# Kernel tuning notes

Hardware: AMD Instinct MI355X
Metric: run time of the kernel (lower is better)

## Reference

```python
import math
import jax, jax.numpy as jnp
import numpy as np

THETA = 10000.0

def _rope_rotate(x, pos):
    # x: [N,H,T,d] with d even; pos: [T] (int or float positions)
    d = x.shape[-1]
    freqs = THETA ** (-jnp.arange(0, d, 2, dtype=jnp.float32) / d)      # [d/2]
    ang = pos.astype(jnp.float32)[:, None] * freqs                       # [T, d/2]
    cos, sin = jnp.cos(ang), jnp.sin(ang)                                # broadcast over N,H
    x1, x2 = x[..., 0::2], x[..., 1::2]                                  # interleaved pairs
    r1 = x1 * cos - x2 * sin
    r2 = x1 * sin + x2 * cos
    return jnp.stack([r1, r2], axis=-1).reshape(x.shape)

def _apply_rope_2d(q, k, pos_h, pos_w):
    # axial 2D RoPE: first half of head_dim rotated by pos_h, second half by pos_w
    dh = q.shape[-1]
    half = dh // 2
    q = jnp.concatenate([_rope_rotate(q[..., :half], pos_h),
                         _rope_rotate(q[..., half:], pos_w)], axis=-1)
    k = jnp.concatenate([_rope_rotate(k[..., :half], pos_h),
                         _rope_rotate(k[..., half:], pos_w)], axis=-1)
    return q, k

def setup_inputs() -> dict:
    key = jax.random.key(0)
    ks = jax.random.split(key, 6)
    N, T, D, H = 4, 2048, 512, 8
    GH, GW = 64, 32  # 64x32 token grid, GH*GW == T
    x = jax.random.normal(ks[0], (N, T, D), dtype=jnp.float32)
    idx = jnp.arange(T, dtype=jnp.int32)
    pos_h = idx // GW
    pos_w = idx % GW
    scale_in = 1.0 / math.sqrt(D)
    w_qkv = jax.random.normal(ks[1], (D, 3 * D), dtype=jnp.float32) * scale_in
    w_proj = jax.random.normal(ks[2], (D, D), dtype=jnp.float32) * scale_in
    b_proj = jnp.zeros((D,), dtype=jnp.float32)
    return {"x": x, "pos_h": pos_h, "pos_w": pos_w,
            "w_qkv": w_qkv, "w_proj": w_proj, "b_proj": b_proj}

def reference(x, pos_h, pos_w, w_qkv, w_proj, b_proj):
    N, T, D = x.shape
    H = 8
    Dh = D // H
    qkv = x @ w_qkv                                   # [N,T,3D]
    q, k, v = jnp.split(qkv, 3, axis=-1)
    def to_heads(t):
        return t.reshape(N, T, H, Dh).transpose(0, 2, 1, 3)  # [N,H,T,Dh]
    q, k, v = to_heads(q), to_heads(k), to_heads(v)
    q, k = _apply_rope_2d(q, k, pos_h, pos_w)
    attn = jnp.einsum('nhtd,nhsd->nhts', q, k) * (1.0 / math.sqrt(Dh))  # [N,H,T,T]
    p = jax.nn.softmax(attn, axis=-1)
    o = jnp.einsum('nhts,nhsd->nhtd', p, v)           # [N,H,T,Dh]
    o = o.transpose(0, 2, 1, 3).reshape(N, T, D)
    return o @ w_proj + b_proj
```

## Files before the change

### kernel.cpp

```cpp
#include <hip/hip_runtime.h>

typedef __attribute__((ext_vector_type(4))) float f32x4;
typedef __attribute__((ext_vector_type(8))) _Float16 f16x8;
typedef __attribute__((ext_vector_type(2))) __fp16 fp16x2_raw;
typedef __attribute__((ext_vector_type(4))) unsigned int u32x4;
typedef __attribute__((ext_vector_type(2))) unsigned int u32x2;

#define MFMA_F16(a, b, c) __builtin_amdgcn_mfma_f32_16x16x32_f16((a), (b), (c), 0, 0, 0)

__device__ __forceinline__ unsigned int pkrtz(float a, float b) {
  union { fp16x2_raw h; unsigned int u; } v;
  v.h = __builtin_amdgcn_cvt_pkrtz(a, b);
  return v.u;
}

__device__ __forceinline__ float fexp2(float x) {
#if __has_builtin(__builtin_amdgcn_exp2f)
  return __builtin_amdgcn_exp2f(x);
#else
  float r;
  asm("v_exp_f32 %0, %1" : "=v"(r) : "v"(x));
  return r;
#endif
}
__device__ __forceinline__ float fsin_rev(float x) {
#if __has_builtin(__builtin_amdgcn_sinf)
  return __builtin_amdgcn_sinf(x);
#else
  float r; asm("v_sin_f32 %0, %1" : "=v"(r) : "v"(x)); return r;
#endif
}
__device__ __forceinline__ float fcos_rev(float x) {
#if __has_builtin(__builtin_amdgcn_cosf)
  return __builtin_amdgcn_cosf(x);
#else
  float r; asm("v_cos_f32 %0, %1" : "=v"(r) : "v"(x)); return r;
#endif
}

typedef const __attribute__((address_space(1))) unsigned int ga_u32_t;
typedef __attribute__((address_space(3))) unsigned int ls_u32_t;
__device__ __forceinline__ void gload16(const void* g, void* l) {
  __builtin_amdgcn_global_load_lds((ga_u32_t*)g, (ls_u32_t*)l, 16, 0, 0);
}

__device__ __forceinline__ void inv_swz64(int seg, int lane, int& r, int& ch) {
  int r_hi = seg * 8 + (lane >> 3);
  int r0 = ((lane >> 2) & 1) ^ ((r_hi >> 1) & 1);
  r = (r_hi << 1) | r0;
  ch = (lane & 3) ^ (r & 3);
}

__global__ __launch_bounds__(256)
void k_prep_x(const float* __restrict__ in, _Float16* __restrict__ out) {
  int i = (blockIdx.x * 256 + threadIdx.x) * 4;
  f32x4 v = *(const f32x4*)(in + i);
  u32x2 p;
  p.x = pkrtz(v[0], v[1]);
  p.y = pkrtz(v[2], v[3]);
  *(u32x2*)(out + i) = p;
}

__global__ __launch_bounds__(256)
void k_prep_w(const float* __restrict__ in, _Float16* __restrict__ out, int N) {
  __shared__ float t[64][65];
  const int tid = threadIdx.x;
  const int bn = blockIdx.x * 64, bk = blockIdx.y * 64;
  #pragma unroll
  for (int it = 0; it < 16; ++it) {
    int idx = it * 256 + tid;
    int kk = idx >> 6, nn = idx & 63;
    t[kk][nn] = in[(bk + kk) * N + bn + nn];
  }
  __syncthreads();
  #pragma unroll
  for (int it = 0; it < 16; ++it) {
    int idx = it * 256 + tid;
    int nn = idx >> 6, kk = idx & 63;
    out[(bn + nn) * 512 + bk + kk] = (_Float16)t[kk][nn];
  }
}

__global__ __launch_bounds__(256, 3)
void k_gemm_qkv(const _Float16* __restrict__ xh,
                const _Float16* __restrict__ wT,
                const int* __restrict__ pos_h,
                const int* __restrict__ pos_w,
                _Float16* __restrict__ qh,
                _Float16* __restrict__ kh,
                _Float16* __restrict__ vT) {
  __shared__ char As[8192], Bs[8192];
  const int tid = threadIdx.x;
  const int lane = tid & 63, w = tid >> 6;
  const int lr = lane & 15, g = lane >> 4;
  const int m0 = blockIdx.y * 128;
  const int n0 = blockIdx.x * 128;
  const int wr = w >> 1, wc = w & 1;

  const _Float16* asrc[2];
  const _Float16* bsrc[2];
  #pragma unroll
  for (int c = 0; c < 2; ++c) {
    int seg = w * 2 + c, r, ch;
    inv_swz64(seg, lane, r, ch);
    asrc[c] = xh + (size_t)(m0 + r) * 512 + ch * 8;
    bsrc[c] = wT + (size_t)(n0 + r) * 512 + ch * 8;
  }

  f32x4 acc[4][4];
  #pragma unroll
  for (int i = 0; i < 4; ++i)
    #pragma unroll
    for (int j = 0; j < 4; ++j) acc[i][j] = (f32x4){0.f, 0.f, 0.f, 0.f};

  for (int kt = 0; kt < 16; ++kt) {
    const int k0 = kt * 32;
    __syncthreads();
    #pragma unroll
    for (int c = 0; c < 2; ++c) {
      gload16(asrc[c] + k0, As + (w * 2 + c) * 1024);
      gload16(bsrc[c] + k0, Bs + (w * 2 + c) * 1024);
    }
    __syncthreads();

    f16x8 af[4], bf[4];
    #pragma unroll
    for (int mi = 0; mi < 4; ++mi) {
      int r = 64 * wr + 16 * mi + lr;
      af[mi] = *(const f16x8*)(As + (((r << 6) + (g << 4)) ^ ((r & 7) << 4)));
    }
    #pragma unroll
    for (int nj = 0; nj < 4; ++nj) {
      int r = 64 * wc + 16 * nj + lr;
      bf[nj] = *(const f16x8*)(Bs + (((r << 6) + (g << 4)) ^ ((r & 7) << 4)));
    }
    __builtin_amdgcn_s_setprio(1);
    #pragma unroll
    for (int mi = 0; mi < 4; ++mi)
      #pragma unroll
      for (int nj = 0; nj < 4; ++nj)
        acc[mi][nj] = MFMA_F16(af[mi], bf[nj], acc[mi][nj]);
    __builtin_amdgcn_s_setprio(0);
  }

  #pragma unroll
  for (int mi = 0; mi < 4; ++mi) {
    const int r0f = m0 + 64 * wr + 16 * mi + 4 * g;
    const int n = r0f >> 11;
    const int t = r0f & 2047;
    #pragma unroll
    for (int nj = 0; nj < 4; ++nj) {
      const int c = n0 + 64 * wc + 16 * nj + lr;
      const int mat = c >> 9;
      const int hh = (c >> 6) & 7;
      const int dh = c & 63;
      f32x4 v = acc[mi][nj];
      if (mat == 2) {
        int tperm = (t & ~31) + 8 * ((t >> 2) & 3) + 4 * ((t >> 4) & 1);
        u32x2 pk2;
        pk2.x = pkrtz(v[0], v[1]);
        pk2.y = pkrtz(v[2], v[3]);
        *(u32x2*)(vT + (size_t)((n * 8 + hh) * 64 + dh) * 2048 + tperm) = pk2;
      } else {
        const int p = (dh & 31) >> 1;
        const float freq_rev = fexp2((float)p * -0.8304820237218405f) * 0.15915494309189535f;
        const int odd = lane & 1;
        const int* posArr = (dh < 32) ? pos_h : pos_w;
        _Float16* dst = mat ? kh : qh;
        const float scale = mat ? 1.0f : 0.125f * 1.44269504088896f;
        #pragma unroll
        for (int i = 0; i < 4; ++i) {
          float val = v[i];
          float oth = __shfl_xor(val, 1);
          float ar = (float)posArr[t + i] * freq_rev;
          ar = ar - floorf(ar);
          float sv = fsin_rev(ar);
          float cv = fcos_rev(ar);
          float x1 = odd ? oth : val;
          float x2 = odd ? val : oth;
          float res = odd ? (x1 * sv + x2 * cv) : (x1 * cv - x2 * sv);
          dst[(size_t)((n * 8 + hh) * 2048 + t + i) * 64 + dh] = (_Float16)(res * scale);
        }
      }
    }
  }
}

__global__ __launch_bounds__(256, 2)
void k_attn(const _Float16* __restrict__ qh,
            const _Float16* __restrict__ kh,
            const _Float16* __restrict__ vp,
            _Float16* __restrict__ o_flat) {
  __shared__ char Ks[2][16384];
  __shared__ char Vs[2][16384];
  const int tid = threadIdx.x, lane = tid & 63, w = tid >> 6;
  const int lr = lane & 15, g = lane >> 4;
  const int bid = blockIdx.x;
  const int qt = (bid >> 3) & 15;
  const int nh = (bid & 7) + 8 * (bid >> 7);

  f16x8 qf[2][2];
  const _Float16* qbase = qh + ((size_t)nh * 2048 + qt * 128 + w * 32) * 64;
  #pragma unroll
  for (int mi = 0; mi < 2; ++mi)
    #pragma unroll
    for (int kg = 0; kg < 2; ++kg)
      qf[mi][kg] = *(const f16x8*)(qbase + (16 * mi + lr) * 64 + kg * 32 + g * 8);

  f16x8 ones;
  #pragma unroll
  for (int i = 0; i < 8; ++i) ones[i] = (_Float16)1.0f;

  f32x4 oacc[2][4];
  f32x4 lacc4[2];
  #pragma unroll
  for (int mi = 0; mi < 2; ++mi) {
    lacc4[mi] = (f32x4){0.f, 0.f, 0.f, 0.f};
    #pragma unroll
    for (int nf = 0; nf < 4; ++nf) oacc[mi][nf] = (f32x4){0.f, 0.f, 0.f, 0.f};
  }

  const _Float16* kb = kh + (size_t)nh * 2048 * 64;
  const _Float16* vb = vp + (size_t)nh * 64 * 2048;

  const int rr = lane >> 3, cc = lane & 7;
  const _Float16* ksrc[2];
  const _Float16* vsrc[2];
  #pragma unroll
  for (int c = 0; c < 2; ++c) {
    int seg = w * 2 + c;
    int r = seg * 8 + rr;
    ksrc[c] = kb + (size_t)r * 64 + ((cc ^ (r & 7)) << 3);
    vsrc[c] = vb + (size_t)r * 2048 + ((cc ^ (r & 7)) << 3);
  }
  auto stage = [&](int b, int kt2) {
    #pragma unroll
    for (int h = 0; h < 2; ++h) {
      int kt = kt2 * 2 + h;
      #pragma unroll
      for (int c = 0; c < 2; ++c) {
        int seg = w * 2 + c;
        gload16(ksrc[c] + (size_t)kt * 4096, Ks[b] + h * 8192 + seg * 1024);
        gload16(vsrc[c] + (size_t)kt * 64,   Vs[b] + h * 8192 + seg * 1024);
      }
    }
  };

  stage(0, 0);

  const f32x4 cinit = (f32x4){-8.f, -8.f, -8.f, -8.f};

  for (int kt2 = 0; kt2 < 16; ++kt2) {
    const int cur = kt2 & 1;
    asm volatile("" ::: "memory");
    __builtin_amdgcn_s_barrier();
    if (kt2 + 1 < 16) {
      stage(cur ^ 1, kt2 + 1);
      asm volatile("s_waitcnt vmcnt(8)" ::: "memory");
    } else {
      asm volatile("s_waitcnt vmcnt(0)" ::: "memory");
    }
    __builtin_amdgcn_s_barrier();
    asm volatile("" ::: "memory");

    f32x4 sacc[2][2][4];
    #pragma unroll
    for (int h = 0; h < 2; ++h)
      #pragma unroll
      for (int mi = 0; mi < 2; ++mi)
        #pragma unroll
        for (int sj = 0; sj < 4; ++sj) sacc[h][mi][sj] = cinit;

    __builtin_amdgcn_s_setprio(1);
    #pragma unroll
    for (int h = 0; h < 2; ++h) {
      const char* Kb = Ks[cur] + h * 8192;
      #pragma unroll
      for (int sj = 0; sj < 4; ++sj) {
        int s = sj * 16 + lr;
        int rb = s << 7, sw = (s & 7) << 4;
        #pragma unroll
        for (int kg = 0; kg < 2; ++kg) {
          f16x8 kf = *(const f16x8*)(Kb + ((rb + (kg << 6) + (g << 4)) ^ sw));
          sacc[h][0][sj] = MFMA_F16(kf, qf[0][kg], sacc[h][0][sj]);
          sacc[h][1][sj] = MFMA_F16(kf, qf[1][kg], sacc[h][1][sj]);
        }
      }
    }
    __builtin_amdgcn_s_setprio(0);

    #pragma unroll
    for (int h = 0; h < 2; ++h) {
      const char* Vb = Vs[cur] + h * 8192;
      #pragma unroll
      for (int mi = 0; mi < 2; ++mi)
        #pragma unroll
        for (int sj = 0; sj < 4; ++sj) {
          sacc[h][mi][sj][0] = fexp2(sacc[h][mi][sj][0]);
          sacc[h][mi][sj][1] = fexp2(sacc[h][mi][sj][1]);
          sacc[h][mi][sj][2] = fexp2(sacc[h][mi][sj][2]);
          sacc[h][mi][sj][3] = fexp2(sacc[h][mi][sj][3]);
        }
      __builtin_amdgcn_s_setprio(1);
      #pragma unroll
      for (int t = 0; t < 2; ++t) {
        f16x8 vf[4];
        #pragma unroll
        for (int nf = 0; nf < 4; ++nf) {
          int dh = 16 * nf + lr;
          vf[nf] = *(const f16x8*)(Vb + (((dh << 7) + (t << 6) + (g << 4)) ^ ((dh & 7) << 4)));
        }
        #pragma unroll
        for (int mi = 0; mi < 2; ++mi) {
          union { unsigned int u[4]; f16x8 h; } pb;
          pb.u[0] = pkrtz(sacc[h][mi][2 * t][0], sacc[h][mi][2 * t][1]);
          pb.u[1] = pkrtz(sacc[h][mi][2 * t][2], sacc[h][mi][2 * t][3]);
          pb.u[2] = pkrtz(sacc[h][mi][2 * t + 1][0], sacc[h][mi][2 * t + 1][1]);
          pb.u[3] = pkrtz(sacc[h][mi][2 * t + 1][2], sacc[h][mi][2 * t + 1][3]);
          lacc4[mi] = MFMA_F16(ones, pb.h, lacc4[mi]);
          #pragma unroll
          for (int nf = 0; nf < 4; ++nf)
            oacc[mi][nf] = MFMA_F16(vf[nf], pb.h, oacc[mi][nf]);
        }
      }
      __builtin_amdgcn_s_setprio(0);
    }
  }

  const int n = nh >> 3, h2 = nh & 7;
  #pragma unroll
  for (int mi = 0; mi < 2; ++mi) {
    float inv = 1.0f / lacc4[mi][0];
    int row = qt * 128 + w * 32 + 16 * mi + lr;
    _Float16* orow = o_flat + ((size_t)(n * 2048 + row)) * 512 + h2 * 64;
    #pragma unroll
    for (int nf = 0; nf < 4; ++nf) {
      u32x2 pk2;
      pk2.x = pkrtz(oacc[mi][nf][0] * inv, oacc[mi][nf][1] * inv);
      pk2.y = pkrtz(oacc[mi][nf][2] * inv, oacc[mi][nf][3] * inv);
      *(u32x2*)(orow + 16 * nf + 4 * g) = pk2;
    }
  }
}

__global__ __launch_bounds__(256, 3)
void k_gemm_proj(const _Float16* __restrict__ o_flat,
                 const _Float16* __restrict__ wpT,
                 const float* __restrict__ bias,
                 float* __restrict__ out) {
  __shared__ char As[8192], Bs[8192];
  const int tid = threadIdx.x;
  const int lane = tid & 63, w = tid >> 6;
  const int lr = lane & 15, g = lane >> 4;
  const int m0 = blockIdx.y * 128;
  const int n0 = blockIdx.x * 128;
  const int wr = w >> 1, wc = w & 1;

  const _Float16* asrc[2];
  const _Float16* bsrc[2];
  #pragma unroll
  for (int c = 0; c < 2; ++c) {
    int seg = w * 2 + c, r, ch;
    inv_swz64(seg, lane, r, ch);
    asrc[c] = o_flat + (size_t)(m0 + r) * 512 + ch * 8;
    bsrc[c] = wpT + (size_t)(n0 + r) * 512 + ch * 8;
  }

  f32x4 acc[4][4];
  #pragma unroll
  for (int i = 0; i < 4; ++i)
    #pragma unroll
    for (int j = 0; j < 4; ++j) acc[i][j] = (f32x4){0.f, 0.f, 0.f, 0.f};

  for (int kt = 0; kt < 16; ++kt) {
    const int k0 = kt * 32;
    __syncthreads();
    #pragma unroll
    for (int c = 0; c < 2; ++c) {
      gload16(asrc[c] + k0, As + (w * 2 + c) * 1024);
      gload16(bsrc[c] + k0, Bs + (w * 2 + c) * 1024);
    }
    __syncthreads();

    f16x8 af[4], bf[4];
    #pragma unroll
    for (int mi = 0; mi < 4; ++mi) {
      int r = 64 * wr + 16 * mi + lr;
      af[mi] = *(const f16x8*)(As + (((r << 6) + (g << 4)) ^ ((r & 7) << 4)));
    }
    #pragma unroll
    for (int nj = 0; nj < 4; ++nj) {
      int r = 64 * wc + 16 * nj + lr;
      bf[nj] = *(const f16x8*)(Bs + (((r << 6) + (g << 4)) ^ ((r & 7) << 4)));
    }
    __builtin_amdgcn_s_setprio(1);
    #pragma unroll
    for (int mi = 0; mi < 4; ++mi)
      #pragma unroll
      for (int nj = 0; nj < 4; ++nj)
        acc[mi][nj] = MFMA_F16(af[mi], bf[nj], acc[mi][nj]);
    __builtin_amdgcn_s_setprio(0);
  }

  #pragma unroll
  for (int mi = 0; mi < 4; ++mi) {
    int r0f = m0 + 64 * wr + 16 * mi + 4 * g;
    #pragma unroll
    for (int nj = 0; nj < 4; ++nj) {
      int c = n0 + 64 * wc + 16 * nj + lr;
      float b = bias[c];
      #pragma unroll
      for (int i = 0; i < 4; ++i)
        out[(size_t)(r0f + i) * 512 + c] = acc[mi][nj][i] + b;
    }
  }
}

extern "C" void kernel_launch(void* const* d_in, const int* in_sizes, int n_in,
                              void* d_out, int out_size, void* d_ws, size_t ws_size,
                              hipStream_t stream) {
  const float* x      = (const float*)d_in[0];
  const int*   pos_h  = (const int*)d_in[1];
  const int*   pos_w  = (const int*)d_in[2];
  const float* w_qkv  = (const float*)d_in[3];
  const float* w_proj = (const float*)d_in[4];
  const float* b_proj = (const float*)d_in[5];
  float* out = (float*)d_out;

  char* ws = (char*)d_ws;
  size_t off = 0;
  auto alloc = [&](size_t bytes) {
    char* p = ws + off;
    off += (bytes + 1023) & ~(size_t)1023;
    return p;
  };
  _Float16* xh     = (_Float16*)alloc((size_t)8192 * 512 * 2);
  _Float16* qh     = (_Float16*)alloc((size_t)32 * 2048 * 64 * 2);
  _Float16* kh     = (_Float16*)alloc((size_t)32 * 2048 * 64 * 2);
  _Float16* vT     = (_Float16*)alloc((size_t)32 * 2048 * 64 * 2);
  _Float16* o_flat = (_Float16*)alloc((size_t)8192 * 512 * 2);
  _Float16* wqT    = (_Float16*)alloc((size_t)1536 * 512 * 2);
  _Float16* wpT    = (_Float16*)alloc((size_t)512 * 512 * 2);

  hipLaunchKernelGGL(k_prep_x, dim3(4096), dim3(256), 0, stream, x, xh);
  hipLaunchKernelGGL(k_prep_w, dim3(24, 8), dim3(256), 0, stream, w_qkv, wqT, 1536);
  hipLaunchKernelGGL(k_prep_w, dim3(8, 8), dim3(256), 0, stream, w_proj, wpT, 512);
  hipLaunchKernelGGL(k_gemm_qkv, dim3(12, 64), dim3(256), 0, stream,
                     xh, wqT, pos_h, pos_w, qh, kh, vT);
  hipLaunchKernelGGL(k_attn, dim3(512), dim3(256), 0, stream, qh, kh, vT, o_flat);
  hipLaunchKernelGGL(k_gemm_proj, dim3(4, 64), dim3(256), 0, stream, o_flat, wpT, b_proj, out);
}
```

Baseline: 92.98 us.

## Halve attention query tile, read V directly from global, merge weight prep launches

The attention kernel now processes 64 query rows per block (16 per wave) instead of 128, doubling the grid to 1024 blocks and raising the occupancy hint to 4. V is no longer staged in shared memory; each wave loads V fragments straight from global memory, which halves LDS use and the async copy count. The two weight-transpose launches are merged into one kernel. The trade-off is that K/V reuse per block drops and global/L2 traffic for V rises, with unswizzled, strided V reads on the critical path.

```diff
diff --git a/kernel.cpp b/kernel.cpp
--- a/kernel.cpp
+++ b/kernel.cpp
@@ -62,10 +62,15 @@
 }
 
 __global__ __launch_bounds__(256)
-void k_prep_w(const float* __restrict__ in, _Float16* __restrict__ out, int N) {
+void k_prep_w2(const float* __restrict__ wq, _Float16* __restrict__ wqT,
+               const float* __restrict__ wp, _Float16* __restrict__ wpT) {
   __shared__ float t[64][65];
   const int tid = threadIdx.x;
-  const int bn = blockIdx.x * 64, bk = blockIdx.y * 64;
+  const int bx = blockIdx.x;
+  const float* in = (bx < 24) ? wq : wp;
+  _Float16* out = (bx < 24) ? wqT : wpT;
+  const int N = (bx < 24) ? 1536 : 512;
+  const int bn = ((bx < 24) ? bx : bx - 24) * 64, bk = blockIdx.y * 64;
   #pragma unroll
   for (int it = 0; it < 16; ++it) {
     int idx = it * 256 + tid;
@@ -186,52 +191,43 @@
   }
 }
 
-__global__ __launch_bounds__(256, 2)
+__global__ __launch_bounds__(256, 4)
 void k_attn(const _Float16* __restrict__ qh,
             const _Float16* __restrict__ kh,
             const _Float16* __restrict__ vp,
             _Float16* __restrict__ o_flat) {
   __shared__ char Ks[2][16384];
-  __shared__ char Vs[2][16384];
   const int tid = threadIdx.x, lane = tid & 63, w = tid >> 6;
   const int lr = lane & 15, g = lane >> 4;
   const int bid = blockIdx.x;
-  const int qt = (bid >> 3) & 15;
-  const int nh = (bid & 7) + 8 * (bid >> 7);
-
-  f16x8 qf[2][2];
-  const _Float16* qbase = qh + ((size_t)nh * 2048 + qt * 128 + w * 32) * 64;
-  #pragma unroll
-  for (int mi = 0; mi < 2; ++mi)
-    #pragma unroll
-    for (int kg = 0; kg < 2; ++kg)
-      qf[mi][kg] = *(const f16x8*)(qbase + (16 * mi + lr) * 64 + kg * 32 + g * 8);
+  const int qt = (bid >> 3) & 31;
+  const int nh = (bid & 7) + 8 * (bid >> 8);
+
+  f16x8 qf[2];
+  const _Float16* qbase = qh + ((size_t)nh * 2048 + qt * 64 + w * 16) * 64;
+  #pragma unroll
+  for (int kg = 0; kg < 2; ++kg)
+    qf[kg] = *(const f16x8*)(qbase + lr * 64 + kg * 32 + g * 8);
 
   f16x8 ones;
   #pragma unroll
   for (int i = 0; i < 8; ++i) ones[i] = (_Float16)1.0f;
 
-  f32x4 oacc[2][4];
-  f32x4 lacc4[2];
-  #pragma unroll
-  for (int mi = 0; mi < 2; ++mi) {
-    lacc4[mi] = (f32x4){0.f, 0.f, 0.f, 0.f};
-    #pragma unroll
-    for (int nf = 0; nf < 4; ++nf) oacc[mi][nf] = (f32x4){0.f, 0.f, 0.f, 0.f};
-  }
+  f32x4 oacc[4];
+  f32x4 lacc4 = (f32x4){0.f, 0.f, 0.f, 0.f};
+  #pragma unroll
+  for (int nf = 0; nf < 4; ++nf) oacc[nf] = (f32x4){0.f, 0.f, 0.f, 0.f};
 
   const _Float16* kb = kh + (size_t)nh * 2048 * 64;
   const _Float16* vb = vp + (size_t)nh * 64 * 2048;
 
   const int rr = lane >> 3, cc = lane & 7;
   const _Float16* ksrc[2];
-  const _Float16* vsrc[2];
   #pragma unroll
   for (int c = 0; c < 2; ++c) {
     int seg = w * 2 + c;
     int r = seg * 8 + rr;
     ksrc[c] = kb + (size_t)r * 64 + ((cc ^ (r & 7)) << 3);
-    vsrc[c] = vb + (size_t)r * 2048 + ((cc ^ (r & 7)) << 3);
   }
   auto stage = [&](int b, int kt2) {
     #pragma unroll
@@ -241,7 +237,6 @@
       for (int c = 0; c < 2; ++c) {
         int seg = w * 2 + c;
         gload16(ksrc[c] + (size_t)kt * 4096, Ks[b] + h * 8192 + seg * 1024);
-        gload16(vsrc[c] + (size_t)kt * 64,   Vs[b] + h * 8192 + seg * 1024);
       }
     }
   };
@@ -256,20 +251,18 @@
     __builtin_amdgcn_s_barrier();
     if (kt2 + 1 < 16) {
       stage(cur ^ 1, kt2 + 1);
-      asm volatile("s_waitcnt vmcnt(8)" ::: "memory");
+      asm volatile("s_waitcnt vmcnt(4)" ::: "memory");
     } else {
       asm volatile("s_waitcnt vmcnt(0)" ::: "memory");
     }
     __builtin_amdgcn_s_barrier();
     asm volatile("" ::: "memory");
 
-    f32x4 sacc[2][2][4];
+    f32x4 sacc[2][4];
     #pragma unroll
     for (int h = 0; h < 2; ++h)
       #pragma unroll
-      for (int mi = 0; mi < 2; ++mi)
-        #pragma unroll
-        for (int sj = 0; sj < 4; ++sj) sacc[h][mi][sj] = cinit;
+      for (int sj = 0; sj < 4; ++sj) sacc[h][sj] = cinit;
 
     __builtin_amdgcn_s_setprio(1);
     #pragma unroll
@@ -282,8 +275,7 @@
         #pragma unroll
         for (int kg = 0; kg < 2; ++kg) {
           f16x8 kf = *(const f16x8*)(Kb + ((rb + (kg << 6) + (g << 4)) ^ sw));
-          sacc[h][0][sj] = MFMA_F16(kf, qf[0][kg], sacc[h][0][sj]);
-          sacc[h][1][sj] = MFMA_F16(kf, qf[1][kg], sacc[h][1][sj]);
+          sacc[h][sj] = MFMA_F16(kf, qf[kg], sacc[h][sj]);
         }
       }
     }
@@ -291,55 +283,47 @@
 
     #pragma unroll
     for (int h = 0; h < 2; ++h) {
-      const char* Vb = Vs[cur] + h * 8192;
-      #pragma unroll
-      for (int mi = 0; mi < 2; ++mi)
-        #pragma unroll
-        for (int sj = 0; sj < 4; ++sj) {
-          sacc[h][mi][sj][0] = fexp2(sacc[h][mi][sj][0]);
-          sacc[h][mi][sj][1] = fexp2(sacc[h][mi][sj][1]);
-          sacc[h][mi][sj][2] = fexp2(sacc[h][mi][sj][2]);
-          sacc[h][mi][sj][3] = fexp2(sacc[h][mi][sj][3]);
-        }
-      __builtin_amdgcn_s_setprio(1);
+      const _Float16* vgb = vb + (size_t)kt2 * 128 + h * 64;
+      #pragma unroll
+      for (int sj = 0; sj < 4; ++sj) {
+        sacc[h][sj][0] = fexp2(sacc[h][sj][0]);
+        sacc[h][sj][1] = fexp2(sacc[h][sj][1]);
+        sacc[h][sj][2] = fexp2(sacc[h][sj][2]);
+        sacc[h][sj][3] = fexp2(sacc[h][sj][3]);
+      }
       #pragma unroll
       for (int t = 0; t < 2; ++t) {
         f16x8 vf[4];
         #pragma unroll
         for (int nf = 0; nf < 4; ++nf) {
           int dh = 16 * nf + lr;
-          vf[nf] = *(const f16x8*)(Vb + (((dh << 7) + (t << 6) + (g << 4)) ^ ((dh & 7) << 4)));
+          vf[nf] = *(const f16x8*)(vgb + (size_t)dh * 2048 + t * 32 + g * 8);
         }
+        union { unsigned int u[4]; f16x8 h; } pb;
+        pb.u[0] = pkrtz(sacc[h][2 * t][0], sacc[h][2 * t][1]);
+        pb.u[1] = pkrtz(sacc[h][2 * t][2], sacc[h][2 * t][3]);
+        pb.u[2] = pkrtz(sacc[h][2 * t + 1][0], sacc[h][2 * t + 1][1]);
+        pb.u[3] = pkrtz(sacc[h][2 * t + 1][2], sacc[h][2 * t + 1][3]);
+        __builtin_amdgcn_s_setprio(1);
+        lacc4 = MFMA_F16(ones, pb.h, lacc4);
         #pragma unroll
-        for (int mi = 0; mi < 2; ++mi) {
-          union { unsigned int u[4]; f16x8 h; } pb;
-          pb.u[0] = pkrtz(sacc[h][mi][2 * t][0], sacc[h][mi][2 * t][1]);
-          pb.u[1] = pkrtz(sacc[h][mi][2 * t][2], sacc[h][mi][2 * t][3]);
-          pb.u[2] = pkrtz(sacc[h][mi][2 * t + 1][0], sacc[h][mi][2 * t + 1][1]);
-          pb.u[3] = pkrtz(sacc[h][mi][2 * t + 1][2], sacc[h][mi][2 * t + 1][3]);
-          lacc4[mi] = MFMA_F16(ones, pb.h, lacc4[mi]);
-          #pragma unroll
-          for (int nf = 0; nf < 4; ++nf)
-            oacc[mi][nf] = MFMA_F16(vf[nf], pb.h, oacc[mi][nf]);
-        }
+        for (int nf = 0; nf < 4; ++nf)
+          oacc[nf] = MFMA_F16(vf[nf], pb.h, oacc[nf]);
+        __builtin_amdgcn_s_setprio(0);
       }
-      __builtin_amdgcn_s_setprio(0);
     }
   }
 
   const int n = nh >> 3, h2 = nh & 7;
-  #pragma unroll
-  for (int mi = 0; mi < 2; ++mi) {
-    float inv = 1.0f / lacc4[mi][0];
-    int row = qt * 128 + w * 32 + 16 * mi + lr;
-    _Float16* orow = o_flat + ((size_t)(n * 2048 + row)) * 512 + h2 * 64;
-    #pragma unroll
-    for (int nf = 0; nf < 4; ++nf) {
-      u32x2 pk2;
-      pk2.x = pkrtz(oacc[mi][nf][0] * inv, oacc[mi][nf][1] * inv);
-      pk2.y = pkrtz(oacc[mi][nf][2] * inv, oacc[mi][nf][3] * inv);
-      *(u32x2*)(orow + 16 * nf + 4 * g) = pk2;
-    }
+  float inv = 1.0f / lacc4[0];
+  int row = qt * 64 + w * 16 + lr;
+  _Float16* orow = o_flat + ((size_t)(n * 2048 + row)) * 512 + h2 * 64;
+  #pragma unroll
+  for (int nf = 0; nf < 4; ++nf) {
+    u32x2 pk2;
+    pk2.x = pkrtz(oacc[nf][0] * inv, oacc[nf][1] * inv);
+    pk2.y = pkrtz(oacc[nf][2] * inv, oacc[nf][3] * inv);
+    *(u32x2*)(orow + 16 * nf + 4 * g) = pk2;
   }
 }
 
@@ -443,10 +427,9 @@
   _Float16* wpT    = (_Float16*)alloc((size_t)512 * 512 * 2);
 
   hipLaunchKernelGGL(k_prep_x, dim3(4096), dim3(256), 0, stream, x, xh);
-  hipLaunchKernelGGL(k_prep_w, dim3(24, 8), dim3(256), 0, stream, w_qkv, wqT, 1536);
-  hipLaunchKernelGGL(k_prep_w, dim3(8, 8), dim3(256), 0, stream, w_proj, wpT, 512);
+  hipLaunchKernelGGL(k_prep_w2, dim3(32, 8), dim3(256), 0, stream, w_qkv, wqT, w_proj, wpT);
   hipLaunchKernelGGL(k_gemm_qkv, dim3(12, 64), dim3(256), 0, stream,
                      xh, wqT, pos_h, pos_w, qh, kh, vT);
-  hipLaunchKernelGGL(k_attn, dim3(512), dim3(256), 0, stream, qh, kh, vT, o_flat);
+  hipLaunchKernelGGL(k_attn, dim3(1024), dim3(256), 0, stream, qh, kh, vT, o_flat);
   hipLaunchKernelGGL(k_gemm_proj, dim3(4, 64), dim3(256), 0, stream, o_flat, wpT, b_proj, out);
 }
```

Result: slower. 176.9 us (+90.2%).

## Merge prep kernels and single-buffer V in attention for higher occupancy

Applied to the files above, without the earlier changes.

Fuses the three fp32-to-fp16 prep launches into one kernel that dispatches on block index, removing two launches. In the attention kernel, V is now single-buffered and loaded at the start of each iteration alongside the next K tile, which cuts LDS per block so three blocks can fit per CU (launch bounds raised to 3). The V load is no longer prefetched an iteration ahead, so it is exposed during the QK^T phase, trading prefetch depth for occupancy and adding register pressure risk.

```diff
diff --git a/kernel.cpp b/kernel.cpp
--- a/kernel.cpp
+++ b/kernel.cpp
@@ -52,20 +52,27 @@
 }
 
 __global__ __launch_bounds__(256)
-void k_prep_x(const float* __restrict__ in, _Float16* __restrict__ out) {
-  int i = (blockIdx.x * 256 + threadIdx.x) * 4;
-  f32x4 v = *(const f32x4*)(in + i);
-  u32x2 p;
-  p.x = pkrtz(v[0], v[1]);
-  p.y = pkrtz(v[2], v[3]);
-  *(u32x2*)(out + i) = p;
-}
-
-__global__ __launch_bounds__(256)
-void k_prep_w(const float* __restrict__ in, _Float16* __restrict__ out, int N) {
+void k_prep(const float* __restrict__ x, _Float16* __restrict__ xh,
+            const float* __restrict__ wq, _Float16* __restrict__ wqT,
+            const float* __restrict__ wp, _Float16* __restrict__ wpT) {
+  const int b = blockIdx.x;
+  const int tid = threadIdx.x;
+  if (b < 4096) {
+    int i = (b * 256 + tid) * 4;
+    f32x4 v = *(const f32x4*)(x + i);
+    u32x2 p;
+    p.x = pkrtz(v[0], v[1]);
+    p.y = pkrtz(v[2], v[3]);
+    *(u32x2*)(xh + i) = p;
+    return;
+  }
   __shared__ float t[64][65];
-  const int tid = threadIdx.x;
-  const int bn = blockIdx.x * 64, bk = blockIdx.y * 64;
+  const int wb = b - 4096;
+  const int bx = wb & 31, by = wb >> 5;
+  const float* in = (bx < 24) ? wq : wp;
+  _Float16* out = (bx < 24) ? wqT : wpT;
+  const int N = (bx < 24) ? 1536 : 512;
+  const int bn = ((bx < 24) ? bx : bx - 24) * 64, bk = by * 64;
   #pragma unroll
   for (int it = 0; it < 16; ++it) {
     int idx = it * 256 + tid;
@@ -186,13 +193,13 @@
   }
 }
 
-__global__ __launch_bounds__(256, 2)
+__global__ __launch_bounds__(256, 3)
 void k_attn(const _Float16* __restrict__ qh,
             const _Float16* __restrict__ kh,
             const _Float16* __restrict__ vp,
             _Float16* __restrict__ o_flat) {
   __shared__ char Ks[2][16384];
-  __shared__ char Vs[2][16384];
+  __shared__ char Vs[16384];
   const int tid = threadIdx.x, lane = tid & 63, w = tid >> 6;
   const int lr = lane & 15, g = lane >> 4;
   const int bid = blockIdx.x;
@@ -233,20 +240,26 @@
     ksrc[c] = kb + (size_t)r * 64 + ((cc ^ (r & 7)) << 3);
     vsrc[c] = vb + (size_t)r * 2048 + ((cc ^ (r & 7)) << 3);
   }
-  auto stage = [&](int b, int kt2) {
+  auto stageK = [&](int b, int kt2) {
     #pragma unroll
     for (int h = 0; h < 2; ++h) {
       int kt = kt2 * 2 + h;
       #pragma unroll
-      for (int c = 0; c < 2; ++c) {
-        int seg = w * 2 + c;
-        gload16(ksrc[c] + (size_t)kt * 4096, Ks[b] + h * 8192 + seg * 1024);
-        gload16(vsrc[c] + (size_t)kt * 64,   Vs[b] + h * 8192 + seg * 1024);
-      }
+      for (int c = 0; c < 2; ++c)
+        gload16(ksrc[c] + (size_t)kt * 4096, Ks[b] + h * 8192 + (w * 2 + c) * 1024);
     }
   };
-
-  stage(0, 0);
+  auto stageV = [&](int kt2) {
+    #pragma unroll
+    for (int h = 0; h < 2; ++h) {
+      int kt = kt2 * 2 + h;
+      #pragma unroll
+      for (int c = 0; c < 2; ++c)
+        gload16(vsrc[c] + (size_t)kt * 64, Vs + h * 8192 + (w * 2 + c) * 1024);
+    }
+  };
+
+  stageK(0, 0);
 
   const f32x4 cinit = (f32x4){-8.f, -8.f, -8.f, -8.f};
 
@@ -254,9 +267,10 @@
     const int cur = kt2 & 1;
     asm volatile("" ::: "memory");
     __builtin_amdgcn_s_barrier();
+    stageV(kt2);
     if (kt2 + 1 < 16) {
-      stage(cur ^ 1, kt2 + 1);
-      asm volatile("s_waitcnt vmcnt(8)" ::: "memory");
+      stageK(cur ^ 1, kt2 + 1);
+      asm volatile("s_waitcnt vmcnt(4)" ::: "memory");
     } else {
       asm volatile("s_waitcnt vmcnt(0)" ::: "memory");
     }
@@ -291,7 +305,7 @@
 
     #pragma unroll
     for (int h = 0; h < 2; ++h) {
-      const char* Vb = Vs[cur] + h * 8192;
+      const char* Vb = Vs + h * 8192;
       #pragma unroll
       for (int mi = 0; mi < 2; ++mi)
         #pragma unroll
@@ -442,9 +456,8 @@
   _Float16* wqT    = (_Float16*)alloc((size_t)1536 * 512 * 2);
   _Float16* wpT    = (_Float16*)alloc((size_t)512 * 512 * 2);
 
-  hipLaunchKernelGGL(k_prep_x, dim3(4096), dim3(256), 0, stream, x, xh);
-  hipLaunchKernelGGL(k_prep_w, dim3(24, 8), dim3(256), 0, stream, w_qkv, wqT, 1536);
-  hipLaunchKernelGGL(k_prep_w, dim3(8, 8), dim3(256), 0, stream, w_proj, wpT, 512);
+  hipLaunchKernelGGL(k_prep, dim3(4352), dim3(256), 0, stream,
+                     x, xh, w_qkv, wqT, w_proj, wpT);
   hipLaunchKernelGGL(k_gemm_qkv, dim3(12, 64), dim3(256), 0, stream,
                      xh, wqT, pos_h, pos_w, qh, kh, vT);
   hipLaunchKernelGGL(k_attn, dim3(512), dim3(256), 0, stream, qh, kh, vT, o_flat);
```

Result: faster. 89.59 us (median of 2 runs) (-3.6%).
